# Optimization experiments

Hardware: AMD Instinct MI355X
Metric: run time of the kernel (lower is better)

Reference implementation:

```python
import jax, jax.numpy as jnp
import numpy as np

F4_E2M1_MAX = 6.0
F8E4M3_MAX = 448.0
E4M3_EPS = 0.015625  # torch.finfo(float8_e4m3fn).tiny = 2**-6
BLOCK = 16
KE2M1 = jnp.array([0.0, 0.5, 1.0, 1.5, 2.0, 3.0, 4.0, 6.0], dtype=jnp.float32)


def round_to_e4m3(x):
    # emulate cast to float8_e4m3fn and back (round-to-nearest-even)
    return x.astype(jnp.float8_e4m3fn).astype(jnp.float32)


def fp4_121_positive(x):
    step1 = jnp.round(2.0 * x) / 2.0   # subnormal-ish region [0,2): step 0.5
    step2 = jnp.round(x)               # [2,4): step 1
    step3 = 2.0 * jnp.round(x / 2.0)   # [4,6]: step 2
    return jnp.where(x < 2.0, step1, jnp.where(x < 4.0, step2, step3))


def cast_to_fp4(x):
    return jnp.sign(x) * fp4_121_positive(jnp.abs(x))


def unpack_fp4_from_uint8(a, m, n):
    # a: int-typed tensor holding byte values in [0,256); two fp4 codes per byte
    high = (a.reshape(-1) >> 4) & 0xF
    low = a.reshape(-1) & 0xF
    combined = jnp.stack((low, high), axis=1).reshape(m, n)  # interleave low,high
    signs = (combined & 8) != 0
    abs_idx = combined & 7
    return KE2M1[abs_idx] * jnp.where(signs, -1.0, 1.0)


def dequant_nvfp4_packed(data_lp, out_scales, per_tensor_scale):
    m, half_n = data_lp.shape
    n = half_n * 2
    data_hp = unpack_fp4_from_uint8(data_lp, m, n)           # [m, n] float32
    scale_fp = out_scales / per_tensor_scale                  # [m, n/16]
    data_hp = data_hp.reshape(m, -1, BLOCK) * scale_fp.reshape(m, -1, 1)
    return data_hp.reshape(m, n)


def qdq_nvfp4(x):
    m, n = x.shape
    tensor_amax = jnp.max(jnp.abs(x))
    pts = jnp.clip(tensor_amax / F8E4M3_MAX, E4M3_EPS, F8E4M3_MAX)  # per-tensor scale
    xb = x.reshape(m, -1, BLOCK)
    block_scale = jnp.max(jnp.abs(xb), axis=-1) / F4_E2M1_MAX       # [m, n/16]
    scaled_bs = round_to_e4m3(jnp.clip(block_scale / pts, E4M3_EPS, F8E4M3_MAX))
    total_scale = pts * scaled_bs                                   # [m, n/16]
    data_scaled = jnp.clip(xb / total_scale[..., None], -F4_E2M1_MAX, F4_E2M1_MAX)
    data_lp = cast_to_fp4(data_scaled)                              # unpacked fp4 values
    # dequant: out_scales / (1/pts) == scaled_bs * pts == total_scale
    return (data_lp * total_scale[..., None]).reshape(m, n)


def setup_inputs() -> dict:
    key = jax.random.key(0)
    k1, k2, k3 = jax.random.split(key, 3)
    M, K, N = 16384, 2048, 2048  # tokens, in_features, out_features
    x = jax.random.normal(k1, (M, K), dtype=jnp.float32)
    weight_packed = jax.random.randint(k2, (N, K // 2), 0, 256, dtype=jnp.int32)
    # fp8-representable positive block scales
    weight_scale = round_to_e4m3(jax.random.uniform(k3, (N, K // 16), dtype=jnp.float32,
                                                    minval=0.05, maxval=1.0))
    weight_global_scale = jnp.ones((1,), dtype=jnp.float32)
    return {"x": x, "weight_packed": weight_packed,
            "weight_scale": weight_scale, "weight_global_scale": weight_global_scale}


def reference(x, weight_packed, weight_scale, weight_global_scale):
    hp_weight = dequant_nvfp4_packed(weight_packed, weight_scale, weight_global_scale)
    x_dq = qdq_nvfp4(x)
    return x_dq @ hp_weight.T
```

## Files before the change

kernel.cpp:

```cpp
#include <hip/hip_runtime.h>

typedef unsigned short u16;
typedef unsigned int u32;
typedef __attribute__((ext_vector_type(8))) short short8;
typedef __attribute__((ext_vector_type(4))) float floatx4;

static constexpr int M = 16384, N = 2048, K = 2048;


__device__ inline u16 f32_to_bf16(float x) {
    u32 u = __float_as_uint(x);
    u += 0x7FFFu + ((u >> 16) & 1u);
    return (u16)(u >> 16);
}

__device__ inline float e4m3_rne(float x) {
    u32 u = __float_as_uint(x);
    u += 0x7FFFFu + ((u >> 20) & 1u);
    u &= 0xFFF00000u;
    return __uint_as_float(u);
}

__device__ inline float fp4_dec(u32 c) {
    u32 e = (c >> 1) & 3u;
    float m = (float)(c & 1u);
    float v = e ? (2.0f + m) * (float)(1u << e) * 0.25f : 0.5f * m;
    return (c & 8u) ? -v : v;
}

__device__ inline float fp4_round_mag(float a) {
    if (a < 2.0f) return rintf(2.0f * a) * 0.5f;
    if (a < 4.0f) return rintf(a);
    return 2.0f * rintf(a * 0.5f);
}

__device__ inline float pts_from_amax(float amax) {
    return fminf(fmaxf(amax / 448.0f, 0.015625f), 448.0f);
}


__global__ void amax_part(const float4* __restrict__ x, float* __restrict__ part, int n4) {
    int idx = blockIdx.x * blockDim.x + threadIdx.x;
    int stride = gridDim.x * blockDim.x;
    float m = 0.0f;
    for (int i = idx; i < n4; i += stride) {
        float4 v = x[i];
        m = fmaxf(m, fmaxf(fmaxf(fabsf(v.x), fabsf(v.y)), fmaxf(fabsf(v.z), fabsf(v.w))));
    }
#pragma unroll
    for (int off = 32; off > 0; off >>= 1)
        m = fmaxf(m, __shfl_down(m, off));
    __shared__ float sm[4];
    if ((threadIdx.x & 63) == 0) sm[threadIdx.x >> 6] = m;
    __syncthreads();
    if (threadIdx.x == 0)
        part[blockIdx.x] = fmaxf(fmaxf(sm[0], sm[1]), fmaxf(sm[2], sm[3]));
}


__global__ void amax_fin(const float* __restrict__ part, u32* __restrict__ out) {
    int t = threadIdx.x;
    float m = fmaxf(part[t], part[t + 1024]);
#pragma unroll
    for (int off = 32; off > 0; off >>= 1)
        m = fmaxf(m, __shfl_down(m, off));
    __shared__ float sm[16];
    if ((t & 63) == 0) sm[t >> 6] = m;
    __syncthreads();
    if (t < 16) {
        m = sm[t];
#pragma unroll
        for (int off = 8; off > 0; off >>= 1)
            m = fmaxf(m, __shfl_down(m, off));
        if (t == 0) *out = __float_as_uint(m);
    }
}


static constexpr int QB = (M * K / 4) / 256;
static constexpr int DB = (N * (K / 2)) / 256;

__global__ void prep(const float4* __restrict__ x, uint2* __restrict__ aq,
                     const u32* __restrict__ amax_bits,
                     const int* __restrict__ wp, const float* __restrict__ wsc,
                     const float* __restrict__ wgs, u16* __restrict__ wq) {
    if (blockIdx.x < QB) {
        int idx = blockIdx.x * blockDim.x + threadIdx.x;
        float4 v = x[idx];

        float bm = fmaxf(fmaxf(fabsf(v.x), fabsf(v.y)), fmaxf(fabsf(v.z), fabsf(v.w)));
        bm = fmaxf(bm, __shfl_xor(bm, 1));
        bm = fmaxf(bm, __shfl_xor(bm, 2));

        float pts = pts_from_amax(__uint_as_float(*amax_bits));
        float bs = bm / 6.0f;
        float sbs = e4m3_rne(fminf(fmaxf(bs / pts, 0.015625f), 448.0f));
        float ts = pts * sbs;

        float vf[4] = {v.x, v.y, v.z, v.w};
        u16 o[4];
#pragma unroll
        for (int i = 0; i < 4; i++) {
            float s = vf[i] / ts;
            s = fminf(fmaxf(s, -6.0f), 6.0f);
            float lp = copysignf(fp4_round_mag(fabsf(s)), s);
            o[i] = f32_to_bf16(lp * sbs);
        }
        aq[idx] = *(const uint2*)o;
    } else {
        int idx = (blockIdx.x - QB) * blockDim.x + threadIdx.x;
        constexpr int Khalf = K / 2;
        int n = idx >> 10;
        int kb = idx & (Khalf - 1);
        u32 byte = (u32)wp[idx] & 0xFFu;
        float scale = wsc[(size_t)n * (K / 16) + (kb >> 3)] / wgs[0];
        float lo = fp4_dec(byte & 0xFu) * scale;
        float hi = fp4_dec((byte >> 4) & 0xFu) * scale;
        u32 out = (u32)f32_to_bf16(lo) | ((u32)f32_to_bf16(hi) << 16);
        ((u32*)wq)[idx] = out;
    }
}


#define GLDS(g, l)                                                              \
    __builtin_amdgcn_global_load_lds(                                           \
        (const __attribute__((address_space(1))) unsigned int*)(g),             \
        (__attribute__((address_space(3))) unsigned int*)(l), 16, 0, 0)

__device__ inline void compute_slab(const u16* __restrict__ sA,
                                    const u16* __restrict__ sB,
                                    floatx4 acc[8][4]) {
    short8 af[8], bf[4];
#pragma unroll
    for (int i = 0; i < 8; i++) af[i] = *(const short8*)(sA + i * 512);
#pragma unroll
    for (int j = 0; j < 4; j++) bf[j] = *(const short8*)(sB + j * 512);
#pragma unroll
    for (int i = 0; i < 8; i++)
#pragma unroll
        for (int j = 0; j < 4; j++)
            acc[i][j] = __builtin_amdgcn_mfma_f32_16x16x32_bf16(
                af[i], bf[j], acc[i][j], 0, 0, 0);
}

__global__ __launch_bounds__(512, 2) void gemm_bt(
    const u16* __restrict__ A, const u16* __restrict__ B,
    float* __restrict__ C, const u32* __restrict__ amax_bits)
{
    __shared__ u16 lA[4][256 * 32];
    __shared__ u16 lB[4][256 * 32];
    constexpr int SLOT = 256 * 32;

    const int tid = threadIdx.x;
    const int w = tid >> 6, lane = tid & 63;

    const int id = blockIdx.x;
    const int xcd = id & 7;
    const int local = id >> 3;
    const int bm = xcd * 8 + (local >> 3);
    const int bn = local & 7;

    const int wm = w >> 2, wn = w & 3;
    const int r16 = lane & 15, q = lane >> 4;

    floatx4 acc[8][4] = {};

    const int srow = lane >> 2;
    const int sq8 = (lane & 3) * 8;
    const u16* gA0 = A + (size_t)(bm * 256 + (w * 2 + 0) * 16 + srow) * K + sq8;
    const u16* gA1 = A + (size_t)(bm * 256 + (w * 2 + 1) * 16 + srow) * K + sq8;
    const u16* gB0 = B + (size_t)(bn * 256 + (w * 2 + 0) * 16 + srow) * K + sq8;
    const u16* gB1 = B + (size_t)(bn * 256 + (w * 2 + 1) * 16 + srow) * K + sq8;
    u16* dA0 = &lA[0][(w * 2 + 0) * 512];
    u16* dA1 = &lA[0][(w * 2 + 1) * 512];
    u16* dB0 = &lB[0][(w * 2 + 0) * 512];
    u16* dB1 = &lB[0][(w * 2 + 1) * 512];

#define STAGE(u) do {                                                          \
        const int _s = (u) & 3; const int _kt = (u) * 32;                      \
        GLDS(gA0 + _kt, dA0 + _s * SLOT);                                      \
        GLDS(gA1 + _kt, dA1 + _s * SLOT);                                      \
        GLDS(gB0 + _kt, dB0 + _s * SLOT);                                      \
        GLDS(gB1 + _kt, dB1 + _s * SLOT);                                      \
    } while (0)

    const u16* sAb = &lA[0][(wm * 128 + r16) * 32 + q * 8];
    const u16* sBb = &lB[0][(wn * 64 + r16) * 32 + q * 8];

    constexpr int NT = K / 32;

    STAGE(0); STAGE(1); STAGE(2);

#pragma unroll 1
    for (int t = 0; t < NT - 3; ++t) {
        asm volatile("s_waitcnt vmcnt(8)" ::: "memory");
        __builtin_amdgcn_s_barrier();
        __builtin_amdgcn_sched_barrier(0);
        STAGE(t + 3);
        const int s = t & 3;
        compute_slab(sAb + s * SLOT, sBb + s * SLOT, acc);
    }
    asm volatile("s_waitcnt vmcnt(8)" ::: "memory");
    __builtin_amdgcn_s_barrier();
    __builtin_amdgcn_sched_barrier(0);
    compute_slab(sAb + ((NT - 3) & 3) * SLOT, sBb + ((NT - 3) & 3) * SLOT, acc);
    asm volatile("s_waitcnt vmcnt(4)" ::: "memory");
    __builtin_amdgcn_s_barrier();
    __builtin_amdgcn_sched_barrier(0);
    compute_slab(sAb + ((NT - 2) & 3) * SLOT, sBb + ((NT - 2) & 3) * SLOT, acc);
    asm volatile("s_waitcnt vmcnt(0)" ::: "memory");
    __builtin_amdgcn_s_barrier();
    __builtin_amdgcn_sched_barrier(0);
    compute_slab(sAb + ((NT - 1) & 3) * SLOT, sBb + ((NT - 1) & 3) * SLOT, acc);

    float pts = pts_from_amax(__uint_as_float(*amax_bits));

    float* Cb = C + (size_t)(bm * 256 + wm * 128 + q * 4) * N
                  + bn * 256 + wn * 64 + r16;
#pragma unroll
    for (int i = 0; i < 8; i++)
#pragma unroll
        for (int j = 0; j < 4; j++)
#pragma unroll
            for (int t = 0; t < 4; t++)
                Cb[(size_t)(i * 16 + t) * N + j * 16] = pts * acc[i][j][t];
}


extern "C" void kernel_launch(void* const* d_in, const int* in_sizes, int n_in,
                              void* d_out, int out_size, void* d_ws, size_t ws_size,
                              hipStream_t stream) {
    const float* x   = (const float*)d_in[0];
    const int*   wp  = (const int*)d_in[1];
    const float* wsc = (const float*)d_in[2];
    const float* wgs = (const float*)d_in[3];
    float* out = (float*)d_out;

    u32*   amax_ws = (u32*)d_ws;
    float* part    = (float*)((char*)d_ws + 64);
    u16*   aq      = (u16*)((char*)d_ws + 16384);
    u16*   wq      = aq + (size_t)M * K;

    amax_part<<<2048, 256, 0, stream>>>((const float4*)x, part, M * K / 4);
    amax_fin<<<1, 1024, 0, stream>>>(part, amax_ws);
    prep<<<QB + DB, 256, 0, stream>>>((const float4*)x, (uint2*)aq, amax_ws,
                                      wp, wsc, wgs, wq);
    gemm_bt<<<(M / 256) * (N / 256), 512, 0, stream>>>(aq, wq, out, amax_ws);
}
```

Baseline: 458.3 us.

## Restructure GEMM mainloop into 8-phase ping-pong schedule with swizzled LDS

Replaces the 4-stage K=32 slab pipeline with K=64 tiles held in two LDS buffers, split into A/B halves. The main loop runs eight phases that interleave LDS fragment reads, global-to-LDS loads of sub-tiles and MFMA quadrants, using setprio and barriers. It also XOR-swizzles the LDS layout to cut bank conflicts. The aim is to overlap memory traffic with MFMA work and cut per-slab barrier overhead. The cost is more barriers per iteration, more complex wait counting, and redundant clamped loads in the last iteration.

```diff
diff --git a/kernel.cpp b/kernel.cpp
--- a/kernel.cpp
+++ b/kernel.cpp
@@ -127,29 +127,11 @@
         (const __attribute__((address_space(1))) unsigned int*)(g),             \
         (__attribute__((address_space(3))) unsigned int*)(l), 16, 0, 0)
 
-__device__ inline void compute_slab(const u16* __restrict__ sA,
-                                    const u16* __restrict__ sB,
-                                    floatx4 acc[8][4]) {
-    short8 af[8], bf[4];
-#pragma unroll
-    for (int i = 0; i < 8; i++) af[i] = *(const short8*)(sA + i * 512);
-#pragma unroll
-    for (int j = 0; j < 4; j++) bf[j] = *(const short8*)(sB + j * 512);
-#pragma unroll
-    for (int i = 0; i < 8; i++)
-#pragma unroll
-        for (int j = 0; j < 4; j++)
-            acc[i][j] = __builtin_amdgcn_mfma_f32_16x16x32_bf16(
-                af[i], bf[j], acc[i][j], 0, 0, 0);
-}
-
 __global__ __launch_bounds__(512, 2) void gemm_bt(
     const u16* __restrict__ A, const u16* __restrict__ B,
     float* __restrict__ C, const u32* __restrict__ amax_bits)
 {
-    __shared__ u16 lA[4][256 * 32];
-    __shared__ u16 lB[4][256 * 32];
-    constexpr int SLOT = 256 * 32;
+    __shared__ u16 sh[2][2][2][8192];
 
     const int tid = threadIdx.x;
     const int w = tid >> 6, lane = tid & 63;
@@ -165,53 +147,85 @@
 
     floatx4 acc[8][4] = {};
 
-    const int srow = lane >> 2;
-    const int sq8 = (lane & 3) * 8;
-    const u16* gA0 = A + (size_t)(bm * 256 + (w * 2 + 0) * 16 + srow) * K + sq8;
-    const u16* gA1 = A + (size_t)(bm * 256 + (w * 2 + 1) * 16 + srow) * K + sq8;
-    const u16* gB0 = B + (size_t)(bn * 256 + (w * 2 + 0) * 16 + srow) * K + sq8;
-    const u16* gB1 = B + (size_t)(bn * 256 + (w * 2 + 1) * 16 + srow) * K + sq8;
-    u16* dA0 = &lA[0][(w * 2 + 0) * 512];
-    u16* dA1 = &lA[0][(w * 2 + 1) * 512];
-    u16* dB0 = &lB[0][(w * 2 + 0) * 512];
-    u16* dB1 = &lB[0][(w * 2 + 1) * 512];
-
-#define STAGE(u) do {                                                          \
-        const int _s = (u) & 3; const int _kt = (u) * 32;                      \
-        GLDS(gA0 + _kt, dA0 + _s * SLOT);                                      \
-        GLDS(gA1 + _kt, dA1 + _s * SLOT);                                      \
-        GLDS(gB0 + _kt, dB0 + _s * SLOT);                                      \
-        GLDS(gB1 + _kt, dB1 + _s * SLOT);                                      \
-    } while (0)
-
-    const u16* sAb = &lA[0][(wm * 128 + r16) * 32 + q * 8];
-    const u16* sBb = &lB[0][(wn * 64 + r16) * 32 + q * 8];
-
-    constexpr int NT = K / 32;
-
-    STAGE(0); STAGE(1); STAGE(2);
+    const int swz = (r16 & 7) << 4;
+    const int aoff0 = r16 * 64 + (((q * 16) ^ swz) >> 1);
+    const int aoff1 = r16 * 64 + (((64 + q * 16) ^ swz) >> 1);
+
+    const int srow8 = lane >> 3;
+    const int scol = ((lane & 7) ^ srow8) * 8;
+    const u16* gA[2], * gB[2];
+    gA[0] = A + (size_t)(bm * 256 + (w * 2 + 0) * 8 + srow8) * K + scol;
+    gA[1] = A + (size_t)(bm * 256 + (w * 2 + 1) * 8 + srow8) * K + scol;
+    gB[0] = B + (size_t)(bn * 256 + (w * 2 + 0) * 8 + srow8) * K + scol;
+    gB[1] = B + (size_t)(bn * 256 + (w * 2 + 1) * 8 + srow8) * K + scol;
+
+#define STG(buf, mat, half, ktc) do {                                           \
+        const u16* _s0 = ((mat) ? gB[0] : gA[0]) + (size_t)(half) * 128 * K + (ktc); \
+        const u16* _s1 = ((mat) ? gB[1] : gA[1]) + (size_t)(half) * 128 * K + (ktc); \
+        GLDS(_s0, &sh[buf][mat][half][w * 1024]);                               \
+        GLDS(_s1, &sh[buf][mat][half][w * 1024 + 512]);                         \
+    } while (0)
+
+    short8 aF[4][2], bF[4][2];
+
+#define RD_A(buf, Qa) do {                                                      \
+        const u16* _ar = &sh[buf][0][wm][(Qa) * 4096];                          \
+        _Pragma("unroll") for (int _i = 0; _i < 4; _i++) {                      \
+            aF[_i][0] = *(const short8*)(_ar + _i * 1024 + aoff0);              \
+            aF[_i][1] = *(const short8*)(_ar + _i * 1024 + aoff1); }            \
+    } while (0)
+
+#define RD_B(buf, Qb) do {                                                      \
+        const u16* _br = &sh[buf][1][wn >> 1][(wn & 1) * 4096 + (Qb) * 2048];   \
+        _Pragma("unroll") for (int _j = 0; _j < 2; _j++) {                      \
+            bF[(Qb) * 2 + _j][0] = *(const short8*)(_br + _j * 1024 + aoff0);   \
+            bF[(Qb) * 2 + _j][1] = *(const short8*)(_br + _j * 1024 + aoff1); } \
+    } while (0)
+
+#define MMA(Qa, Qb) do {                                                        \
+        __builtin_amdgcn_sched_barrier(0);                                      \
+        __builtin_amdgcn_s_barrier();                                           \
+        __builtin_amdgcn_sched_barrier(0);                                      \
+        __builtin_amdgcn_s_setprio(1);                                          \
+        _Pragma("unroll") for (int _i = 0; _i < 4; _i++)                        \
+        _Pragma("unroll") for (int _j = 0; _j < 2; _j++)                        \
+        _Pragma("unroll") for (int _k = 0; _k < 2; _k++)                        \
+            acc[(Qa) * 4 + _i][(Qb) * 2 + _j] =                                 \
+                __builtin_amdgcn_mfma_f32_16x16x32_bf16(                        \
+                    aF[_i][_k], bF[(Qb) * 2 + _j][_k],                          \
+                    acc[(Qa) * 4 + _i][(Qb) * 2 + _j], 0, 0, 0);                \
+        __builtin_amdgcn_s_setprio(0);                                          \
+        __builtin_amdgcn_sched_barrier(0);                                      \
+    } while (0)
+
+#define ENDPH __builtin_amdgcn_s_barrier()
+#define CHK4 do { asm volatile("s_waitcnt vmcnt(4)" ::: "memory");              \
+                  __builtin_amdgcn_sched_barrier(0); } while (0)
+
+    STG(0, 0, 0, 0); STG(0, 0, 1, 0);
+    STG(0, 1, 0, 0); STG(0, 1, 1, 0);
+    STG(1, 1, 0, 64); STG(1, 1, 1, 64);
+    CHK4;
+    __builtin_amdgcn_s_barrier();
 
 #pragma unroll 1
-    for (int t = 0; t < NT - 3; ++t) {
-        asm volatile("s_waitcnt vmcnt(8)" ::: "memory");
-        __builtin_amdgcn_s_barrier();
-        __builtin_amdgcn_sched_barrier(0);
-        STAGE(t + 3);
-        const int s = t & 3;
-        compute_slab(sAb + s * SLOT, sBb + s * SLOT, acc);
-    }
-    asm volatile("s_waitcnt vmcnt(8)" ::: "memory");
-    __builtin_amdgcn_s_barrier();
-    __builtin_amdgcn_sched_barrier(0);
-    compute_slab(sAb + ((NT - 3) & 3) * SLOT, sBb + ((NT - 3) & 3) * SLOT, acc);
-    asm volatile("s_waitcnt vmcnt(4)" ::: "memory");
-    __builtin_amdgcn_s_barrier();
-    __builtin_amdgcn_sched_barrier(0);
-    compute_slab(sAb + ((NT - 2) & 3) * SLOT, sBb + ((NT - 2) & 3) * SLOT, acc);
+    for (int it = 0; it < K / 128; ++it) {
+        const int ktY  = (2 * it + 1) * 64;
+        const int kx2  = 2 * it + 2, ky2 = 2 * it + 3;
+        const int ktX2 = (kx2 <= 31 ? kx2 : 31) * 64;
+        const int ktY2 = (ky2 <= 31 ? ky2 : 31) * 64;
+
+        RD_A(0, 0); RD_B(0, 0); STG(1, 0, 0, ktY);  MMA(0, 0);       ENDPH;
+        RD_B(0, 1);             STG(1, 0, 1, ktY);  MMA(0, 1);       ENDPH;
+        RD_A(0, 1);             STG(0, 1, 0, ktX2); MMA(1, 1);       ENDPH;
+                                STG(0, 1, 1, ktX2); MMA(1, 0); CHK4; ENDPH;
+        RD_A(1, 0); RD_B(1, 0); STG(0, 0, 0, ktX2); MMA(0, 0);       ENDPH;
+        RD_B(1, 1);             STG(0, 0, 1, ktX2); MMA(0, 1);       ENDPH;
+        RD_A(1, 1);             STG(1, 1, 0, ktY2); MMA(1, 1);       ENDPH;
+                                STG(1, 1, 1, ktY2); MMA(1, 0); CHK4; ENDPH;
+    }
+
     asm volatile("s_waitcnt vmcnt(0)" ::: "memory");
-    __builtin_amdgcn_s_barrier();
-    __builtin_amdgcn_sched_barrier(0);
-    compute_slab(sAb + ((NT - 1) & 3) * SLOT, sBb + ((NT - 1) & 3) * SLOT, acc);
 
     float pts = pts_from_amax(__uint_as_float(*amax_bits));
 
```

Result: faster. 378.7 us (-17.4%).
